# Optimization experiments

Measured on AMD Instinct MI355X. Metric: run time of the kernel, lower is better.

The kernel has to match this reference:

```python
import jax, jax.numpy as jnp
import numpy as np

N = 50000        # num_nodes
E = 800000       # num edges (avg degree 16)
R = 8            # num_relations
D_IN = 128       # input_dim
D_H = 128        # gnn_dim
D_OUT = 128      # embed_dim
NUM_DRUGS = 4000 # nodes with node_type == 0 used for pairing
P = 8192         # number of drug pairs (edge_filter columns)


def setup_inputs() -> dict:
    key = jax.random.key(0)
    ks = jax.random.split(key, 24)
    s = 0.05

    def w(k, shape):
        return jax.random.normal(k, shape, jnp.float32) * s

    inp = {
        "x": jax.random.normal(ks[0], (N, D_IN), jnp.float32),
        "edge_index": jax.random.randint(ks[1], (2, E), 0, N),
        "edge_type": jax.random.randint(ks[2], (E,), 0, R),
        "node_type": jax.random.randint(ks[3], (N,), 0, 2),
        "edge_filter": jax.random.randint(ks[4], (2, P), 0, NUM_DRUGS),
        # RGCN layer 1/2/3: per-relation weights, root weight, bias
        "W1": w(ks[5], (R, D_IN, D_H)), "root1": w(ks[6], (D_IN, D_H)), "b1": jnp.zeros((D_H,), jnp.float32),
        "W2": w(ks[7], (R, D_H, D_H)),  "root2": w(ks[8], (D_H, D_H)),  "b2": jnp.zeros((D_H,), jnp.float32),
        "W3": w(ks[9], (R, D_H, D_H)),  "root3": w(ks[10], (D_H, D_H)), "b3": jnp.zeros((D_H,), jnp.float32),
        # ComboMLP: Bilinear(d,d,d) + 3-layer MLP
        "bil_W": w(ks[11], (D_H, D_H, D_H)), "bil_b": jnp.zeros((D_H,), jnp.float32),
        "m1_W": w(ks[12], (D_H, D_H)), "m1_b": jnp.zeros((D_H,), jnp.float32),
        "m2_W": w(ks[13], (D_H, D_H)), "m2_b": jnp.zeros((D_H,), jnp.float32),
        "m3_W": w(ks[14], (D_H, D_OUT)), "m3_b": jnp.zeros((D_OUT,), jnp.float32),
    }
    return inp


def _rgcn_layer(x, src, dst, etype, W, root, b):
    # PyG RGCNConv with aggr='mean': per relation r, mean of neighbor
    # features over incoming rel-r edges, transformed by W[r]; plus root + bias.
    d = x.shape[1]
    msgs = x[src]                                   # [E, d] gather
    seg = dst * R + etype                           # per-(node, relation) segment id
    agg = jax.ops.segment_sum(msgs, seg, num_segments=N * R).reshape(N, R, d)
    cnt = jax.ops.segment_sum(jnp.ones_like(etype, jnp.float32), seg,
                              num_segments=N * R).reshape(N, R, 1)
    mean = agg / jnp.maximum(cnt, 1.0)              # nodes w/o rel-r edges -> 0
    return jnp.einsum('nrd,rde->ne', mean, W) + x @ root + b


def reference(x, edge_index, edge_type, node_type, edge_filter,
              W1, root1, b1, W2, root2, b2, W3, root3, b3,
              bil_W, bil_b, m1_W, m1_b, m2_W, m2_b, m3_W, m3_b):
    src, dst = edge_index[0], edge_index[1]
    h = jax.nn.relu(_rgcn_layer(x, src, dst, edge_type, W1, root1, b1))
    h = jax.nn.relu(_rgcn_layer(h, src, dst, edge_type, W2, root2, b2))
    h = jax.nn.relu(_rgcn_layer(h, src, dst, edge_type, W3, root3, b3))

    # drug_embeds = kg_out[where(node_type == 0)] (fixed-size for jit)
    drug_idx = jnp.nonzero(node_type == 0, size=NUM_DRUGS, fill_value=0)[0]
    drug = h[drug_idx]                              # [NUM_DRUGS, d]
    fa = drug[edge_filter[0]]                       # [P, d]
    fb = drug[edge_filter[1]]                       # [P, d]

    # torch.nn.Bilinear: out[p,o] = fa[p] @ bil_W[o] @ fb[p] + bil_b[o]
    x_ab = jax.nn.relu(jnp.einsum('pi,oij,pj->po', fa, bil_W, fb) + bil_b)
    x_ab = jax.nn.relu(x_ab @ m1_W + m1_b)
    x_ab = jax.nn.relu(x_ab @ m2_W + m2_b)
    return x_ab @ m3_W + m3_b                       # [P, D_OUT]
```

## Files before the change

kernel.cpp:

```cpp
#include <hip/hip_runtime.h>
#include <hip/hip_bf16.h>

typedef unsigned short ushort_t;
typedef __attribute__((ext_vector_type(8))) short short8v;
typedef __attribute__((ext_vector_type(4))) float f32x4;
typedef __attribute__((ext_vector_type(4))) int int4v;

#define NN 50000
#define EE 800000
#define RRR 8
#define DD 128
#define NDRUG 4000
#define PPAIR 8192
#define BML 32
#define AFS 1160

#define XB4   (NN * DD / 4)
#define WCAT1 (144 * 128 * 8)
#define PREP_T (XB4 + 3 * WCAT1 + 3 * 16384 + 2097152)

__device__ __forceinline__ float bf2f(ushort_t u) {
    unsigned int v = ((unsigned int)u) << 16;
    float f; __builtin_memcpy(&f, &v, 4); return f;
}
__device__ __forceinline__ ushort_t f2bf(float f) {
    unsigned int b; __builtin_memcpy(&b, &f, 4);
    unsigned int r = (b + 0x7FFFu + ((b >> 16) & 1u)) >> 16;
    return (ushort_t)r;
}
__device__ __forceinline__ unsigned int pkbf(float lo, float hi) {
    unsigned int r;
    asm("v_cvt_pk_bf16_f32 %0, %1, %2" : "=v"(r) : "v"(lo), "v"(hi));
    return r;
}


__global__ __launch_bounds__(256) void k_count(const int* __restrict__ ei,
                                               const int* __restrict__ et,
                                               int* __restrict__ cnt) {
    int e = blockIdx.x * 256 + threadIdx.x;
    if (e < EE) {
        int dst = ei[EE + e];
        atomicAdd(&cnt[dst * RRR + et[e]], 1);
    }
}

__global__ __launch_bounds__(1024) void k_scanA(const int* __restrict__ cnt,
                                                float* __restrict__ inv,
                                                int* __restrict__ offs,
                                                int* __restrict__ part) {
    __shared__ int ws[16];
    int tid = threadIdx.x, wid = tid >> 6, lane = tid & 63;
    int i = blockIdx.x * 1024 + tid;
    int v0 = 0;
    if (i < NN) {
#pragma unroll
        for (int r = 0; r < RRR; r++) {
            int c = cnt[i * RRR + r];
            v0 += c;
            inv[i * RRR + r] = 1.0f / (float)(c > 0 ? c : 1);
        }
    }
    int v = v0;
#pragma unroll
    for (int off = 1; off < 64; off <<= 1) {
        int u = __shfl_up(v, off);
        if (lane >= off) v += u;
    }
    if (lane == 63) ws[wid] = v;
    __syncthreads();
    if (wid == 0) {
        int wv = (lane < 16) ? ws[lane] : 0;
#pragma unroll
        for (int off = 1; off < 16; off <<= 1) {
            int u = __shfl_up(wv, off);
            if (lane >= off) wv += u;
        }
        if (lane < 16) ws[lane] = wv;
    }
    __syncthreads();
    int excl = (wid ? ws[wid - 1] : 0) + (v - v0);
    if (i < NN) offs[i] = excl;
    if (tid == 0) part[blockIdx.x] = ws[15];
}

__global__ __launch_bounds__(64) void k_scanB(int* __restrict__ part, int nPart) {
    int tid = threadIdx.x;
    int p0 = (tid < nPart) ? part[tid] : 0;
    int p = p0;
#pragma unroll
    for (int off = 1; off < 64; off <<= 1) {
        int u = __shfl_up(p, off);
        if (tid >= off) p += u;
    }
    if (tid < nPart) part[tid] = p - p0;
}

__global__ __launch_bounds__(1024) void k_scanC(int* __restrict__ offs,
                                                const int* __restrict__ part,
                                                int* __restrict__ cursor) {
    int i = blockIdx.x * 1024 + threadIdx.x;
    if (i < NN) {
        int v = offs[i] + part[blockIdx.x];
        offs[i] = v;
        cursor[i] = v;
    }
    if (i == NN) offs[NN] = EE;
}

__global__ __launch_bounds__(1024) void k_select(const int* __restrict__ ntype,
                                                 int* __restrict__ didx) {
    __shared__ int ws[16];
    __shared__ int sbase;
    int tid = threadIdx.x, wid = tid >> 6, lane = tid & 63;
    if (tid == 0) sbase = 0;
    __syncthreads();
    for (int c0 = 0; c0 < NN; c0 += 1024) {
        int i = c0 + tid;
        int v0 = (i < NN && ntype[i] == 0) ? 1 : 0;
        int v = v0;
#pragma unroll
        for (int off = 1; off < 64; off <<= 1) {
            int u = __shfl_up(v, off);
            if (lane >= off) v += u;
        }
        if (lane == 63) ws[wid] = v;
        __syncthreads();
        if (wid == 0) {
            int wv = (lane < 16) ? ws[lane] : 0;
#pragma unroll
            for (int off = 1; off < 16; off <<= 1) {
                int u = __shfl_up(wv, off);
                if (lane >= off) wv += u;
            }
            if (lane < 16) ws[lane] = wv;
        }
        __syncthreads();
        int excl = sbase + (wid ? ws[wid - 1] : 0) + (v - v0);
        if (v0 && excl < NDRUG) didx[excl] = i;
        __syncthreads();
        if (tid == 0) sbase += ws[15];
        __syncthreads();
    }
}

__global__ __launch_bounds__(256) void k_scatter(const int* __restrict__ ei,
                                                 const int* __restrict__ et,
                                                 int* __restrict__ cursor,
                                                 int* __restrict__ sorted) {
    int e = blockIdx.x * 256 + threadIdx.x;
    if (e < EE) {
        int dst = ei[EE + e];
        int pos = atomicAdd(&cursor[dst], 1);
        sorted[pos] = ei[e] | (et[e] << 20);
    }
}

__global__ __launch_bounds__(256) void k_prep(
        const float* __restrict__ x,
        const float* __restrict__ W1, const float* __restrict__ r1,
        const float* __restrict__ W2, const float* __restrict__ r2,
        const float* __restrict__ W3, const float* __restrict__ r3,
        const float* __restrict__ m1W, const float* __restrict__ m2W,
        const float* __restrict__ m3W, const float* __restrict__ bilW,
        ushort_t* __restrict__ xb,
        ushort_t* __restrict__ Wc1, ushort_t* __restrict__ Wc2, ushort_t* __restrict__ Wc3,
        ushort_t* __restrict__ mo1, ushort_t* __restrict__ mo2, ushort_t* __restrict__ mo3,
        ushort_t* __restrict__ Wb3) {
    int idx = blockIdx.x * 256 + threadIdx.x;
    if (idx < XB4) {
        float4 v = ((const float4*)x)[idx];
        uint2 o;
        o.x = (unsigned int)f2bf(v.x) | ((unsigned int)f2bf(v.y) << 16);
        o.y = (unsigned int)f2bf(v.z) | ((unsigned int)f2bf(v.w) << 16);
        ((uint2*)xb)[idx] = o;
    } else if (idx < XB4 + 3 * WCAT1) {
        int t = idx - XB4;
        int l = t / WCAT1, j = t - l * WCAT1;
        const float* W8   = (l == 0) ? W1 : (l == 1) ? W2 : W3;
        const float* root = (l == 0) ? r1 : (l == 1) ? r2 : r3;
        ushort_t* dst     = (l == 0) ? Wc1 : (l == 1) ? Wc2 : Wc3;
        int e = j & 7, col = (j >> 3) & 127, ko = j >> 10;
        int k = ko * 8 + e, slab = k >> 7, kk = k & 127;
        const float* src = (slab < 8) ? (W8 + slab * 16384) : root;
        dst[j] = f2bf(src[kk * 128 + col]);
    } else if (idx < XB4 + 3 * WCAT1 + 3 * 16384) {
        int t = idx - XB4 - 3 * WCAT1;
        int l = t >> 14, j = t & 16383;
        const float* src = (l == 0) ? m1W : (l == 1) ? m2W : m3W;
        ushort_t* dst    = (l == 0) ? mo1 : (l == 1) ? mo2 : mo3;
        int col = j >> 7, kk = j & 127;
        dst[j] = f2bf(src[kk * 128 + col]);
    } else {
        int j = idx - (XB4 + 3 * WCAT1 + 3 * 16384);
        int e = j & 7, o = (j >> 3) & 127, ko = j >> 10;
        Wb3[j] = f2bf(bilW[(size_t)o * 16384 + ko * 8 + e]);
    }
}

__global__ __launch_bounds__(512) void k_layer(const ushort_t* __restrict__ hin,
                                               const ushort_t* __restrict__ WcatT,
                                               const float* __restrict__ bias,
                                               const float* __restrict__ inv,
                                               const int* __restrict__ offs,
                                               const int* __restrict__ sorted,
                                               ushort_t* __restrict__ hout) {
    __shared__ short Af[BML * AFS];
    int tid = threadIdx.x;
    int n0 = blockIdx.x * BML;
    int node = tid >> 4, tsub = tid & 15;
    int n = n0 + node;

    float acc[8][8];
#pragma unroll
    for (int r = 0; r < 8; r++)
#pragma unroll
        for (int q = 0; q < 8; q++) acc[r][q] = 0.f;
    short8v hv = {0, 0, 0, 0, 0, 0, 0, 0};

    if (n < NN) {
        hv = ((const short8v*)hin)[(size_t)n * 16 + tsub];
        int e0 = offs[n], e1 = offs[n + 1];
        const int4v* hg = (const int4v*)hin;
        for (int e = e0; e < e1; e++) {
            int pk = sorted[e];
            int src = pk & 0xFFFFF;
            int et = pk >> 20;
            union { int4v v; short s[8]; } u;
            u.v = hg[(size_t)src * 16 + tsub];
            float v[8];
#pragma unroll
            for (int q = 0; q < 8; q++) v[q] = bf2f((ushort_t)u.s[q]);
#define CASE_R(R) case R: _Pragma("unroll") for (int q = 0; q < 8; q++) acc[R][q] += v[q]; break;
            switch (et) {
                CASE_R(0) CASE_R(1) CASE_R(2) CASE_R(3)
                CASE_R(4) CASE_R(5) CASE_R(6) CASE_R(7)
            }
#undef CASE_R
        }
    }
    int nc = (n < NN) ? n : (NN - 1);
#pragma unroll
    for (int slab = 0; slab < 8; slab++) {
        float sc = (n < NN) ? inv[nc * 8 + slab] : 0.f;
        union { unsigned int u[4]; short8v v; } cv;
        cv.u[0] = pkbf(acc[slab][0] * sc, acc[slab][1] * sc);
        cv.u[1] = pkbf(acc[slab][2] * sc, acc[slab][3] * sc);
        cv.u[2] = pkbf(acc[slab][4] * sc, acc[slab][5] * sc);
        cv.u[3] = pkbf(acc[slab][6] * sc, acc[slab][7] * sc);
        *(short8v*)&Af[node * AFS + slab * 128 + tsub * 8] = cv.v;
    }
    *(short8v*)&Af[node * AFS + 1024 + tsub * 8] = hv;
    __syncthreads();

    int wid = tid >> 6, lane = tid & 63, lo = lane & 15, hi = lane >> 4;
    int rhalf = wid & 1, cgrp = wid >> 1;
    int arow = rhalf * 16 + lo;
    f32x4 a0v = {0.f, 0.f, 0.f, 0.f}, a1v = {0.f, 0.f, 0.f, 0.f};
    const int4v* Bg = (const int4v*)WcatT;
#pragma unroll
    for (int kc = 0; kc < 9; kc++) {
#pragma unroll
        for (int s = 0; s < 4; s++) {
            short8v a = *(const short8v*)&Af[arow * AFS + kc * 128 + s * 32 + hi * 8];
            int ko = kc * 16 + s * 4 + hi;
            union { int4v i; short8v s8; } b0, b1;
            b0.i = Bg[ko * 128 + cgrp * 32 + lo];
            b1.i = Bg[ko * 128 + cgrp * 32 + 16 + lo];
            a0v = __builtin_amdgcn_mfma_f32_16x16x32_bf16(a, b0.s8, a0v, 0, 0, 0);
            a1v = __builtin_amdgcn_mfma_f32_16x16x32_bf16(a, b1.s8, a1v, 0, 0, 0);
        }
    }
#pragma unroll
    for (int q = 0; q < 4; q++) {
        int r = n0 + rhalf * 16 + hi * 4 + q;
        if (r < NN) {
            int c = cgrp * 32 + lo;
            float v0 = fmaxf(a0v[q] + bias[c], 0.f);
            float v1 = fmaxf(a1v[q] + bias[c + 16], 0.f);
            hout[(size_t)r * 128 + c] = f2bf(v0);
            hout[(size_t)r * 128 + c + 16] = f2bf(v1);
        }
    }
}

__global__ __launch_bounds__(256) void k_mfma_nn(const ushort_t* __restrict__ A,
                                                 const ushort_t* __restrict__ Wt,
                                                 const float* __restrict__ bias,
                                                 ushort_t* __restrict__ outb,
                                                 float* __restrict__ outf,
                                                 int M, int nMblk, int relu) {
    __shared__ short As[64 * 136];
    __shared__ short Bs[128 * 136];
    int tid = threadIdx.x;
    int mblk = blockIdx.x % nMblk;
    int row0 = mblk * 64;

    const int4v* Ag = (const int4v*)A;
    int4v* AsV = (int4v*)As;
    for (int idx = tid; idx < 1024; idx += 256) {
        int row = idx >> 4, ck = idx & 15;
        int grow = row0 + row;
        int4v v = {0, 0, 0, 0};
        if (grow < M) v = Ag[(size_t)grow * 16 + ck];
        AsV[row * 17 + ck] = v;
    }
    const int4v* Wg = (const int4v*)Wt;
    int4v* BsV = (int4v*)Bs;
    for (int idx = tid; idx < 2048; idx += 256) {
        int col = idx >> 4, ck = idx & 15;
        BsV[col * 17 + ck] = Wg[idx];
    }
    __syncthreads();

    int wid = tid >> 6, lane = tid & 63, lo = lane & 15, hi = lane >> 4;
    int wrow0 = wid * 16;
    f32x4 acc[8];
#pragma unroll
    for (int t = 0; t < 8; t++) acc[t] = (f32x4)(0.f);

#pragma unroll
    for (int s = 0; s < 4; ++s) {
        short8v a = *(const short8v*)&As[(wrow0 + lo) * 136 + s * 32 + hi * 8];
#pragma unroll
        for (int t = 0; t < 8; t++) {
            short8v b = *(const short8v*)&Bs[(t * 16 + lo) * 136 + s * 32 + hi * 8];
            acc[t] = __builtin_amdgcn_mfma_f32_16x16x32_bf16(a, b, acc[t], 0, 0, 0);
        }
    }

#pragma unroll
    for (int t = 0; t < 8; t++) {
        int col = t * 16 + lo;
        float bs = bias ? bias[col] : 0.f;
#pragma unroll
        for (int q = 0; q < 4; q++) {
            int grow = row0 + wrow0 + hi * 4 + q;
            if (grow < M) {
                float v = acc[t][q] + bs;
                if (relu) v = fmaxf(v, 0.f);
                size_t oidx = (size_t)grow * 128 + col;
                if (outb) outb[oidx] = f2bf(v);
                else      outf[oidx] = v;
            }
        }
    }
}

__global__ __launch_bounds__(512) void k_bil(const ushort_t* __restrict__ hb,
                                             const int* __restrict__ didx,
                                             const int* __restrict__ efil,
                                             const ushort_t* __restrict__ Wb,
                                             const float* __restrict__ bilb,
                                             ushort_t* __restrict__ xab) {
    __shared__ __align__(16) char smem[65536];
    __shared__ int pa[32], pb[32];
    float* faT = (float*)smem;
    float* fbF = (float*)(smem + 16896);
    int tid = threadIdx.x;
    int p0 = blockIdx.x * 32;

    if (tid < 32) pa[tid] = didx[efil[p0 + tid]];
    else if (tid < 64) pb[tid - 32] = didx[efil[PPAIR + p0 + tid - 32]];
    __syncthreads();

    {
        int p = tid >> 4, c8 = tid & 15;
        const int4v* hg = (const int4v*)hb;
        union { int4v v; short s[8]; } ra, rb;
        ra.v = hg[(size_t)pa[p] * 16 + c8];
        rb.v = hg[(size_t)pb[p] * 16 + c8];
        float4* fb4 = (float4*)fbF;
        float4 f0, f1;
        f0.x = bf2f((ushort_t)rb.s[0]); f0.y = bf2f((ushort_t)rb.s[1]);
        f0.z = bf2f((ushort_t)rb.s[2]); f0.w = bf2f((ushort_t)rb.s[3]);
        f1.x = bf2f((ushort_t)rb.s[4]); f1.y = bf2f((ushort_t)rb.s[5]);
        f1.z = bf2f((ushort_t)rb.s[6]); f1.w = bf2f((ushort_t)rb.s[7]);
        fb4[p * 33 + c8 * 2] = f0;
        fb4[p * 33 + c8 * 2 + 1] = f1;
#pragma unroll
        for (int j = 0; j < 8; j++)
            faT[(c8 * 8 + j) * 33 + p] = bf2f((ushort_t)ra.s[j]);
    }
    __syncthreads();

    int wid = tid >> 6, lane = tid & 63, lo = lane & 15, hi = lane >> 4;
    const int4v* Wbg = (const int4v*)Wb;
    const float4* fb4 = (const float4*)fbF;

    f32x4 acc0[8], acc1[8];
#pragma unroll
    for (int t = 0; t < 8; t++) { acc0[t] = (f32x4)(0.f); acc1[t] = (f32x4)(0.f); }

    for (int s = 0; s < 64; ++s) {
        int ko = (wid << 8) + (s << 2) + hi;
        int4v braw[8];
#pragma unroll
        for (int t = 0; t < 8; t++)
            braw[t] = Wbg[ko * 128 + t * 16 + lo];

        int i = (wid << 4) + (s >> 2);
        int jc4 = ((s & 3) << 3) + (hi << 1);
        short8v afr0, afr1;
#pragma unroll
        for (int mi = 0; mi < 2; ++mi) {
            int prow = (mi << 4) + lo;
            float fa = faT[i * 33 + prow];
            float4 f0 = fb4[prow * 33 + jc4];
            float4 f1 = fb4[prow * 33 + jc4 + 1];
            union { unsigned int u[4]; short8v v; } cv;
            cv.u[0] = pkbf(fa * f0.x, fa * f0.y);
            cv.u[1] = pkbf(fa * f0.z, fa * f0.w);
            cv.u[2] = pkbf(fa * f1.x, fa * f1.y);
            cv.u[3] = pkbf(fa * f1.z, fa * f1.w);
            if (mi == 0) afr0 = cv.v; else afr1 = cv.v;
        }
#pragma unroll
        for (int t = 0; t < 8; t++) {
            union { int4v i4; short8v s8; } bb; bb.i4 = braw[t];
            acc0[t] = __builtin_amdgcn_mfma_f32_16x16x32_bf16(afr0, bb.s8, acc0[t], 0, 0, 0);
            acc1[t] = __builtin_amdgcn_mfma_f32_16x16x32_bf16(afr1, bb.s8, acc1[t], 0, 0, 0);
        }
    }
    __syncthreads();

    float* redF = (float*)smem;
    if (wid >= 4) {
        float* r = redF + (wid - 4) * 4096;
#pragma unroll
        for (int t = 0; t < 8; t++)
#pragma unroll
            for (int q = 0; q < 4; q++) {
                r[(hi * 4 + q) * 128 + t * 16 + lo] = acc0[t][q];
                r[(16 + hi * 4 + q) * 128 + t * 16 + lo] = acc1[t][q];
            }
    }
    __syncthreads();
    if (wid < 4) {
        float* r = redF + wid * 4096;
#pragma unroll
        for (int t = 0; t < 8; t++)
#pragma unroll
            for (int q = 0; q < 4; q++) {
                acc0[t][q] += r[(hi * 4 + q) * 128 + t * 16 + lo];
                acc1[t][q] += r[(16 + hi * 4 + q) * 128 + t * 16 + lo];
            }
    }
    __syncthreads();
    if (wid < 4) {
        float* r = redF + wid * 4096;
#pragma unroll
        for (int t = 0; t < 8; t++)
#pragma unroll
            for (int q = 0; q < 4; q++) {
                r[(hi * 4 + q) * 128 + t * 16 + lo] = acc0[t][q];
                r[(16 + hi * 4 + q) * 128 + t * 16 + lo] = acc1[t][q];
            }
    }
    __syncthreads();
    for (int idx = tid; idx < 4096; idx += 512) {
        float s = redF[idx] + redF[4096 + idx] + redF[8192 + idx] + redF[12288 + idx]
                + bilb[idx & 127];
        s = fmaxf(s, 0.f);
        xab[(size_t)(p0 + (idx >> 7)) * 128 + (idx & 127)] = f2bf(s);
    }
}


extern "C" void kernel_launch(void* const* d_in, const int* in_sizes, int n_in,
                              void* d_out, int out_size, void* d_ws, size_t ws_size,
                              hipStream_t stream) {
    const float* x      = (const float*)d_in[0];
    const int*   ei     = (const int*)d_in[1];
    const int*   et     = (const int*)d_in[2];
    const int*   ntype  = (const int*)d_in[3];
    const int*   efil   = (const int*)d_in[4];
    const float* W1 = (const float*)d_in[5];
    const float* r1 = (const float*)d_in[6];
    const float* b1 = (const float*)d_in[7];
    const float* W2 = (const float*)d_in[8];
    const float* r2 = (const float*)d_in[9];
    const float* b2 = (const float*)d_in[10];
    const float* W3 = (const float*)d_in[11];
    const float* r3 = (const float*)d_in[12];
    const float* b3 = (const float*)d_in[13];
    const float* bilW = (const float*)d_in[14];
    const float* bilb = (const float*)d_in[15];
    const float* m1W = (const float*)d_in[16];
    const float* m1b = (const float*)d_in[17];
    const float* m2W = (const float*)d_in[18];
    const float* m2b = (const float*)d_in[19];
    const float* m3W = (const float*)d_in[20];
    const float* m3b = (const float*)d_in[21];
    float* outp = (float*)d_out;

    char* ws = (char*)d_ws;
    size_t off = 0;
    auto alloc = [&](size_t bytes) { size_t c = off; off = (off + bytes + 255) & ~(size_t)255; return c; };

    const int nScanBlk = (NN + 1023) / 1024;

    size_t oxb   = alloc((size_t)NN * 128 * 2);
    size_t ohA   = alloc((size_t)NN * 128 * 2);
    size_t ohB   = alloc((size_t)NN * 128 * 2);
    size_t oWc1  = alloc((size_t)WCAT1 * 2);
    size_t oWc2  = alloc((size_t)WCAT1 * 2);
    size_t oWc3  = alloc((size_t)WCAT1 * 2);
    size_t omW1  = alloc((size_t)16384 * 2);
    size_t omW2  = alloc((size_t)16384 * 2);
    size_t omW3  = alloc((size_t)16384 * 2);
    size_t oWb   = alloc((size_t)2097152 * 2);
    size_t oxab1 = alloc((size_t)PPAIR * 128 * 2);
    size_t oxab2 = alloc((size_t)PPAIR * 128 * 2);
    size_t ocnt  = alloc((size_t)NN * RRR * sizeof(int));
    size_t odidx = alloc((size_t)NDRUG * sizeof(int));
    size_t oinv  = alloc((size_t)NN * RRR * sizeof(float));
    size_t ooffs = alloc((size_t)(NN + 1) * sizeof(int));
    size_t ocur  = alloc((size_t)NN * sizeof(int));
    size_t opart = alloc((size_t)64 * sizeof(int));
    size_t osort = alloc((size_t)EE * sizeof(int));

    ushort_t* xb   = (ushort_t*)(ws + oxb);
    ushort_t* hbA  = (ushort_t*)(ws + ohA);
    ushort_t* hbB  = (ushort_t*)(ws + ohB);
    ushort_t* Wc1  = (ushort_t*)(ws + oWc1);
    ushort_t* Wc2  = (ushort_t*)(ws + oWc2);
    ushort_t* Wc3  = (ushort_t*)(ws + oWc3);
    ushort_t* mWt1 = (ushort_t*)(ws + omW1);
    ushort_t* mWt2 = (ushort_t*)(ws + omW2);
    ushort_t* mWt3 = (ushort_t*)(ws + omW3);
    ushort_t* Wb3  = (ushort_t*)(ws + oWb);
    ushort_t* xab1 = (ushort_t*)(ws + oxab1);
    ushort_t* xab2 = (ushort_t*)(ws + oxab2);
    int*      cnt  = (int*)(ws + ocnt);
    int*      didx = (int*)(ws + odidx);
    float*    inv  = (float*)(ws + oinv);
    int*      offs = (int*)(ws + ooffs);
    int*      cursor = (int*)(ws + ocur);
    int*      part = (int*)(ws + opart);
    int*      sorted = (int*)(ws + osort);

    hipMemsetAsync(cnt, 0, (odidx - ocnt) + (size_t)NDRUG * sizeof(int), stream);

    k_prep<<<(PREP_T + 255) / 256, 256, 0, stream>>>(
        x, W1, r1, W2, r2, W3, r3, m1W, m2W, m3W, bilW,
        xb, Wc1, Wc2, Wc3, mWt1, mWt2, mWt3, Wb3);

    k_count<<<(EE + 255) / 256, 256, 0, stream>>>(ei, et, cnt);
    k_scanA<<<nScanBlk, 1024, 0, stream>>>(cnt, inv, offs, part);
    k_scanB<<<1, 64, 0, stream>>>(part, nScanBlk);
    k_scanC<<<nScanBlk + 1, 1024, 0, stream>>>(offs, part, cursor);
    k_select<<<1, 1024, 0, stream>>>(ntype, didx);
    k_scatter<<<(EE + 255) / 256, 256, 0, stream>>>(ei, et, cursor, sorted);

    const int NBL = (NN + BML - 1) / BML;

    k_layer<<<NBL, 512, 0, stream>>>(xb,  Wc1, b1, inv, offs, sorted, hbA);
    k_layer<<<NBL, 512, 0, stream>>>(hbA, Wc2, b2, inv, offs, sorted, hbB);
    k_layer<<<NBL, 512, 0, stream>>>(hbB, Wc3, b3, inv, offs, sorted, hbA);

    k_bil<<<PPAIR / 32, 512, 0, stream>>>(hbA, didx, efil, Wb3, bilb, xab1);
    const int nMblkP = PPAIR / 64;
    k_mfma_nn<<<nMblkP, 256, 0, stream>>>(xab1, mWt1, m1b, xab2, nullptr, PPAIR, nMblkP, 1);
    k_mfma_nn<<<nMblkP, 256, 0, stream>>>(xab2, mWt2, m2b, xab1, nullptr, PPAIR, nMblkP, 1);
    k_mfma_nn<<<nMblkP, 256, 0, stream>>>(xab1, mWt3, m3b, nullptr, outp, PPAIR, nMblkP, 0);
}
```

Before: 703.3 us.

## Fuse edge counting into prep, merge drug select into scan, widen bilinear tile

Edge counting now runs in the prep kernel's tail threads, and the single-block serial drug-index selection is folded into the parallel multi-block scan through a second prefix sum. This removes two launches and a long serial single-block kernel. The bilinear kernel now processes 64 pairs per block instead of 32, with warps split across two pair halves and four K quarters, so each Wb load is reused over twice as many pairs. The cost is more shared memory and fewer blocks (128) to fill the GPU, and the final reduction is restructured to write directly from registers.

```diff
diff --git a/kernel.cpp b/kernel.cpp
--- a/kernel.cpp
+++ b/kernel.cpp
@@ -34,128 +34,6 @@
     return r;
 }
 
-
-__global__ __launch_bounds__(256) void k_count(const int* __restrict__ ei,
-                                               const int* __restrict__ et,
-                                               int* __restrict__ cnt) {
-    int e = blockIdx.x * 256 + threadIdx.x;
-    if (e < EE) {
-        int dst = ei[EE + e];
-        atomicAdd(&cnt[dst * RRR + et[e]], 1);
-    }
-}
-
-__global__ __launch_bounds__(1024) void k_scanA(const int* __restrict__ cnt,
-                                                float* __restrict__ inv,
-                                                int* __restrict__ offs,
-                                                int* __restrict__ part) {
-    __shared__ int ws[16];
-    int tid = threadIdx.x, wid = tid >> 6, lane = tid & 63;
-    int i = blockIdx.x * 1024 + tid;
-    int v0 = 0;
-    if (i < NN) {
-#pragma unroll
-        for (int r = 0; r < RRR; r++) {
-            int c = cnt[i * RRR + r];
-            v0 += c;
-            inv[i * RRR + r] = 1.0f / (float)(c > 0 ? c : 1);
-        }
-    }
-    int v = v0;
-#pragma unroll
-    for (int off = 1; off < 64; off <<= 1) {
-        int u = __shfl_up(v, off);
-        if (lane >= off) v += u;
-    }
-    if (lane == 63) ws[wid] = v;
-    __syncthreads();
-    if (wid == 0) {
-        int wv = (lane < 16) ? ws[lane] : 0;
-#pragma unroll
-        for (int off = 1; off < 16; off <<= 1) {
-            int u = __shfl_up(wv, off);
-            if (lane >= off) wv += u;
-        }
-        if (lane < 16) ws[lane] = wv;
-    }
-    __syncthreads();
-    int excl = (wid ? ws[wid - 1] : 0) + (v - v0);
-    if (i < NN) offs[i] = excl;
-    if (tid == 0) part[blockIdx.x] = ws[15];
-}
-
-__global__ __launch_bounds__(64) void k_scanB(int* __restrict__ part, int nPart) {
-    int tid = threadIdx.x;
-    int p0 = (tid < nPart) ? part[tid] : 0;
-    int p = p0;
-#pragma unroll
-    for (int off = 1; off < 64; off <<= 1) {
-        int u = __shfl_up(p, off);
-        if (tid >= off) p += u;
-    }
-    if (tid < nPart) part[tid] = p - p0;
-}
-
-__global__ __launch_bounds__(1024) void k_scanC(int* __restrict__ offs,
-                                                const int* __restrict__ part,
-                                                int* __restrict__ cursor) {
-    int i = blockIdx.x * 1024 + threadIdx.x;
-    if (i < NN) {
-        int v = offs[i] + part[blockIdx.x];
-        offs[i] = v;
-        cursor[i] = v;
-    }
-    if (i == NN) offs[NN] = EE;
-}
-
-__global__ __launch_bounds__(1024) void k_select(const int* __restrict__ ntype,
-                                                 int* __restrict__ didx) {
-    __shared__ int ws[16];
-    __shared__ int sbase;
-    int tid = threadIdx.x, wid = tid >> 6, lane = tid & 63;
-    if (tid == 0) sbase = 0;
-    __syncthreads();
-    for (int c0 = 0; c0 < NN; c0 += 1024) {
-        int i = c0 + tid;
-        int v0 = (i < NN && ntype[i] == 0) ? 1 : 0;
-        int v = v0;
-#pragma unroll
-        for (int off = 1; off < 64; off <<= 1) {
-            int u = __shfl_up(v, off);
-            if (lane >= off) v += u;
-        }
-        if (lane == 63) ws[wid] = v;
-        __syncthreads();
-        if (wid == 0) {
-            int wv = (lane < 16) ? ws[lane] : 0;
-#pragma unroll
-            for (int off = 1; off < 16; off <<= 1) {
-                int u = __shfl_up(wv, off);
-                if (lane >= off) wv += u;
-            }
-            if (lane < 16) ws[lane] = wv;
-        }
-        __syncthreads();
-        int excl = sbase + (wid ? ws[wid - 1] : 0) + (v - v0);
-        if (v0 && excl < NDRUG) didx[excl] = i;
-        __syncthreads();
-        if (tid == 0) sbase += ws[15];
-        __syncthreads();
-    }
-}
-
-__global__ __launch_bounds__(256) void k_scatter(const int* __restrict__ ei,
-                                                 const int* __restrict__ et,
-                                                 int* __restrict__ cursor,
-                                                 int* __restrict__ sorted) {
-    int e = blockIdx.x * 256 + threadIdx.x;
-    if (e < EE) {
-        int dst = ei[EE + e];
-        int pos = atomicAdd(&cursor[dst], 1);
-        sorted[pos] = ei[e] | (et[e] << 20);
-    }
-}
-
 __global__ __launch_bounds__(256) void k_prep(
         const float* __restrict__ x,
         const float* __restrict__ W1, const float* __restrict__ r1,
@@ -163,10 +41,11 @@
         const float* __restrict__ W3, const float* __restrict__ r3,
         const float* __restrict__ m1W, const float* __restrict__ m2W,
         const float* __restrict__ m3W, const float* __restrict__ bilW,
+        const int* __restrict__ ei, const int* __restrict__ et,
         ushort_t* __restrict__ xb,
         ushort_t* __restrict__ Wc1, ushort_t* __restrict__ Wc2, ushort_t* __restrict__ Wc3,
         ushort_t* __restrict__ mo1, ushort_t* __restrict__ mo2, ushort_t* __restrict__ mo3,
-        ushort_t* __restrict__ Wb3) {
+        ushort_t* __restrict__ Wb3, int* __restrict__ cnt) {
     int idx = blockIdx.x * 256 + threadIdx.x;
     if (idx < XB4) {
         float4 v = ((const float4*)x)[idx];
@@ -191,10 +70,111 @@
         ushort_t* dst    = (l == 0) ? mo1 : (l == 1) ? mo2 : mo3;
         int col = j >> 7, kk = j & 127;
         dst[j] = f2bf(src[kk * 128 + col]);
-    } else {
+    } else if (idx < PREP_T) {
         int j = idx - (XB4 + 3 * WCAT1 + 3 * 16384);
         int e = j & 7, o = (j >> 3) & 127, ko = j >> 10;
         Wb3[j] = f2bf(bilW[(size_t)o * 16384 + ko * 8 + e]);
+    } else {
+        int e = idx - PREP_T;
+        if (e < EE) {
+            int dst = ei[EE + e];
+            atomicAdd(&cnt[dst * RRR + et[e]], 1);
+        }
+    }
+}
+
+__global__ __launch_bounds__(1024) void k_scanA(const int* __restrict__ cnt,
+                                                const int* __restrict__ ntype,
+                                                float* __restrict__ inv,
+                                                int* __restrict__ offs,
+                                                int* __restrict__ selx,
+                                                int* __restrict__ part,
+                                                int* __restrict__ part2) {
+    __shared__ int w1[16], w2[16];
+    int tid = threadIdx.x, wid = tid >> 6, lane = tid & 63;
+    int i = blockIdx.x * 1024 + tid;
+    int a0 = 0, b0 = 0;
+    if (i < NN) {
+#pragma unroll
+        for (int r = 0; r < RRR; r++) {
+            int c = cnt[i * RRR + r];
+            a0 += c;
+            inv[i * RRR + r] = 1.0f / (float)(c > 0 ? c : 1);
+        }
+        b0 = (ntype[i] == 0) ? 1 : 0;
+    }
+    int a = a0, b = b0;
+#pragma unroll
+    for (int off = 1; off < 64; off <<= 1) {
+        int ua = __shfl_up(a, off);
+        int ub = __shfl_up(b, off);
+        if (lane >= off) { a += ua; b += ub; }
+    }
+    if (lane == 63) { w1[wid] = a; w2[wid] = b; }
+    __syncthreads();
+    if (wid == 0) {
+        int wa = (lane < 16) ? w1[lane] : 0;
+        int wb = (lane < 16) ? w2[lane] : 0;
+#pragma unroll
+        for (int off = 1; off < 16; off <<= 1) {
+            int ua = __shfl_up(wa, off);
+            int ub = __shfl_up(wb, off);
+            if (lane >= off) { wa += ua; wb += ub; }
+        }
+        if (lane < 16) { w1[lane] = wa; w2[lane] = wb; }
+    }
+    __syncthreads();
+    if (i < NN) {
+        offs[i] = (wid ? w1[wid - 1] : 0) + (a - a0);
+        selx[i] = (wid ? w2[wid - 1] : 0) + (b - b0);
+    }
+    if (tid == 0) { part[blockIdx.x] = w1[15]; part2[blockIdx.x] = w2[15]; }
+}
+
+__global__ __launch_bounds__(64) void k_scanB(int* __restrict__ part,
+                                              int* __restrict__ part2, int nPart) {
+    int tid = threadIdx.x;
+    int p0 = (tid < nPart) ? part[tid] : 0;
+    int q0 = (tid < nPart) ? part2[tid] : 0;
+    int p = p0, q = q0;
+#pragma unroll
+    for (int off = 1; off < 64; off <<= 1) {
+        int u = __shfl_up(p, off);
+        int v = __shfl_up(q, off);
+        if (tid >= off) { p += u; q += v; }
+    }
+    if (tid < nPart) { part[tid] = p - p0; part2[tid] = q - q0; }
+}
+
+__global__ __launch_bounds__(1024) void k_scanC(int* __restrict__ offs,
+                                                const int* __restrict__ selx,
+                                                const int* __restrict__ part,
+                                                const int* __restrict__ part2,
+                                                const int* __restrict__ ntype,
+                                                int* __restrict__ cursor,
+                                                int* __restrict__ didx) {
+    int i = blockIdx.x * 1024 + threadIdx.x;
+    if (i < NN) {
+        int v = offs[i] + part[blockIdx.x];
+        offs[i] = v;
+        cursor[i] = v;
+        if (ntype[i] == 0) {
+            int s = selx[i] + part2[blockIdx.x];
+            if (s < NDRUG) didx[s] = i;
+        }
+    }
+    if (i == NN) offs[NN] = EE;
+}
+
+__global__ __launch_bounds__(256) void k_scatter(const int* __restrict__ ei,
+                                                 const int* __restrict__ et,
+                                                 int* __restrict__ cursor,
+                                                 int* __restrict__ sorted) {
+    int e = blockIdx.x * 256 + threadIdx.x;
+    if (e < EE) {
+        int dst = ei[EE + e];
+        int pos = atomicAdd(&cursor[dst], 1);
+        sorted[pos] = ei[e] | (et[e] << 20);
     }
 }
 
@@ -353,19 +333,19 @@
                                              const ushort_t* __restrict__ Wb,
                                              const float* __restrict__ bilb,
                                              ushort_t* __restrict__ xab) {
-    __shared__ __align__(16) char smem[65536];
-    __shared__ int pa[32], pb[32];
+    __shared__ __align__(16) char smem[67072];
+    __shared__ int pa[64], pb[64];
     float* faT = (float*)smem;
-    float* fbF = (float*)(smem + 16896);
+    float* fbF = (float*)(smem + 33280);
     int tid = threadIdx.x;
-    int p0 = blockIdx.x * 32;
-
-    if (tid < 32) pa[tid] = didx[efil[p0 + tid]];
-    else if (tid < 64) pb[tid - 32] = didx[efil[PPAIR + p0 + tid - 32]];
-    __syncthreads();
-
-    {
-        int p = tid >> 4, c8 = tid & 15;
+    int p0 = blockIdx.x * 64;
+
+    if (tid < 64) pa[tid] = didx[efil[p0 + tid]];
+    else if (tid < 128) pb[tid - 64] = didx[efil[PPAIR + p0 + tid - 64]];
+    __syncthreads();
+
+    for (int t = tid; t < 1024; t += 512) {
+        int p = t >> 4, c8 = t & 15;
         const int4v* hg = (const int4v*)hb;
         union { int4v v; short s[8]; } ra, rb;
         ra.v = hg[(size_t)pa[p] * 16 + c8];
@@ -380,11 +360,12 @@
         fb4[p * 33 + c8 * 2 + 1] = f1;
 #pragma unroll
         for (int j = 0; j < 8; j++)
-            faT[(c8 * 8 + j) * 33 + p] = bf2f((ushort_t)ra.s[j]);
+            faT[(c8 * 8 + j) * 65 + p] = bf2f((ushort_t)ra.s[j]);
     }
     __syncthreads();
 
     int wid = tid >> 6, lane = tid & 63, lo = lane & 15, hi = lane >> 4;
+    int ph = wid & 1, kQ = wid >> 1;
     const int4v* Wbg = (const int4v*)Wb;
     const float4* fb4 = (const float4*)fbF;
 
@@ -392,20 +373,20 @@
 #pragma unroll
     for (int t = 0; t < 8; t++) { acc0[t] = (f32x4)(0.f); acc1[t] = (f32x4)(0.f); }
 
-    for (int s = 0; s < 64; ++s) {
-        int ko = (wid << 8) + (s << 2) + hi;
+    for (int s = 0; s < 128; ++s) {
+        int ko = (kQ << 9) + (s << 2) + hi;
         int4v braw[8];
 #pragma unroll
         for (int t = 0; t < 8; t++)
             braw[t] = Wbg[ko * 128 + t * 16 + lo];
 
-        int i = (wid << 4) + (s >> 2);
+        int i = (kQ << 5) + (s >> 2);
         int jc4 = ((s & 3) << 3) + (hi << 1);
         short8v afr0, afr1;
 #pragma unroll
         for (int mi = 0; mi < 2; ++mi) {
-            int prow = (mi << 4) + lo;
-            float fa = faT[i * 33 + prow];
+            int prow = (ph << 5) + (mi << 4) + lo;
+            float fa = faT[i * 65 + prow];
             float4 f0 = fb4[prow * 33 + jc4];
             float4 f1 = fb4[prow * 33 + jc4 + 1];
             union { unsigned int u[4]; short8v v; } cv;
@@ -425,8 +406,8 @@
     __syncthreads();
 
     float* redF = (float*)smem;
-    if (wid >= 4) {
-        float* r = redF + (wid - 4) * 4096;
+    if (kQ >= 2) {
+        float* r = redF + (((kQ - 2) << 1) + ph) * 4096;
 #pragma unroll
         for (int t = 0; t < 8; t++)
 #pragma unroll
@@ -436,8 +417,8 @@
             }
     }
     __syncthreads();
-    if (wid < 4) {
-        float* r = redF + wid * 4096;
+    if (kQ < 2) {
+        float* r = redF + ((kQ << 1) + ph) * 4096;
 #pragma unroll
         for (int t = 0; t < 8; t++)
 #pragma unroll
@@ -447,8 +428,8 @@
             }
     }
     __syncthreads();
-    if (wid < 4) {
-        float* r = redF + wid * 4096;
+    if (kQ == 1) {
+        float* r = redF + ph * 4096;
 #pragma unroll
         for (int t = 0; t < 8; t++)
 #pragma unroll
@@ -458,11 +439,22 @@
             }
     }
     __syncthreads();
-    for (int idx = tid; idx < 4096; idx += 512) {
-        float s = redF[idx] + redF[4096 + idx] + redF[8192 + idx] + redF[12288 + idx]
-                + bilb[idx & 127];
-        s = fmaxf(s, 0.f);
-        xab[(size_t)(p0 + (idx >> 7)) * 128 + (idx & 127)] = f2bf(s);
+    if (kQ == 0) {
+        float* r = redF + ph * 4096;
+#pragma unroll
+        for (int t = 0; t < 8; t++) {
+            int col = t * 16 + lo;
+            float bs = bilb[col];
+#pragma unroll
+            for (int q = 0; q < 4; q++) {
+                float s0 = acc0[t][q] + r[(hi * 4 + q) * 128 + col] + bs;
+                float s1 = acc1[t][q] + r[(16 + hi * 4 + q) * 128 + col] + bs;
+                int pr0 = p0 + (ph << 5) + hi * 4 + q;
+                int pr1 = pr0 + 16;
+                xab[(size_t)pr0 * 128 + col] = f2bf(fmaxf(s0, 0.f));
+                xab[(size_t)pr1 * 128 + col] = f2bf(fmaxf(s1, 0.f));
+            }
+        }
     }
 }
 
@@ -516,8 +508,10 @@
     size_t odidx = alloc((size_t)NDRUG * sizeof(int));
     size_t oinv  = alloc((size_t)NN * RRR * sizeof(float));
     size_t ooffs = alloc((size_t)(NN + 1) * sizeof(int));
+    size_t oselx = alloc((size_t)NN * sizeof(int));
     size_t ocur  = alloc((size_t)NN * sizeof(int));
     size_t opart = alloc((size_t)64 * sizeof(int));
+    size_t opart2 = alloc((size_t)64 * sizeof(int));
     size_t osort = alloc((size_t)EE * sizeof(int));
 
     ushort_t* xb   = (ushort_t*)(ws + oxb);
@@ -536,21 +530,21 @@
     int*      didx = (int*)(ws + odidx);
     float*    inv  = (float*)(ws + oinv);
     int*      offs = (int*)(ws + ooffs);
+    int*      selx = (int*)(ws + oselx);
     int*      cursor = (int*)(ws + ocur);
     int*      part = (int*)(ws + opart);
+    int*      part2 = (int*)(ws + opart2);
     int*      sorted = (int*)(ws + osort);
 
     hipMemsetAsync(cnt, 0, (odidx - ocnt) + (size_t)NDRUG * sizeof(int), stream);
 
-    k_prep<<<(PREP_T + 255) / 256, 256, 0, stream>>>(
-        x, W1, r1, W2, r2, W3, r3, m1W, m2W, m3W, bilW,
-        xb, Wc1, Wc2, Wc3, mWt1, mWt2, mWt3, Wb3);
-
-    k_count<<<(EE + 255) / 256, 256, 0, stream>>>(ei, et, cnt);
-    k_scanA<<<nScanBlk, 1024, 0, stream>>>(cnt, inv, offs, part);
-    k_scanB<<<1, 64, 0, stream>>>(part, nScanBlk);
-    k_scanC<<<nScanBlk + 1, 1024, 0, stream>>>(offs, part, cursor);
-    k_select<<<1, 1024, 0, stream>>>(ntype, didx);
+    k_prep<<<(PREP_T + EE + 255) / 256, 256, 0, stream>>>(
+        x, W1, r1, W2, r2, W3, r3, m1W, m2W, m3W, bilW, ei, et,
+        xb, Wc1, Wc2, Wc3, mWt1, mWt2, mWt3, Wb3, cnt);
+
+    k_scanA<<<nScanBlk, 1024, 0, stream>>>(cnt, ntype, inv, offs, selx, part, part2);
+    k_scanB<<<1, 64, 0, stream>>>(part, part2, nScanBlk);
+    k_scanC<<<nScanBlk + 1, 1024, 0, stream>>>(offs, selx, part, part2, ntype, cursor, didx);
     k_scatter<<<(EE + 255) / 256, 256, 0, stream>>>(ei, et, cursor, sorted);
 
     const int NBL = (NN + BML - 1) / BML;
@@ -559,7 +553,7 @@
     k_layer<<<NBL, 512, 0, stream>>>(hbA, Wc2, b2, inv, offs, sorted, hbB);
     k_layer<<<NBL, 512, 0, stream>>>(hbB, Wc3, b3, inv, offs, sorted, hbA);
 
-    k_bil<<<PPAIR / 32, 512, 0, stream>>>(hbA, didx, efil, Wb3, bilb, xab1);
+    k_bil<<<PPAIR / 64, 512, 0, stream>>>(hbA, didx, efil, Wb3, bilb, xab1);
     const int nMblkP = PPAIR / 64;
     k_mfma_nn<<<nMblkP, 256, 0, stream>>>(xab1, mWt1, m1b, xab2, nullptr, PPAIR, nMblkP, 1);
     k_mfma_nn<<<nMblkP, 256, 0, stream>>>(xab2, mWt2, m2b, xab1, nullptr, PPAIR, nMblkP, 1);
```

Measured after the change: 719.0 us. 2.2% more time.
